# Kernel tuning notes

Hardware: AMD Instinct MI355X
Metric: run time of the kernel (lower is better)

The kernel has to match this reference:

```python
import jax, jax.numpy as jnp
import numpy as np

B, N, C, H = 8, 1025, 1024, 16


def setup_inputs() -> dict:
    key = jax.random.key(0)
    k1, k2, k3, k4 = jax.random.split(key, 4)
    x = jax.random.normal(k1, (B, N, C), dtype=jnp.float32)
    w_qkv = jax.random.normal(k2, (3 * C, C), dtype=jnp.float32) * (C ** -0.5)
    w_proj = jax.random.normal(k3, (C, C), dtype=jnp.float32) * (C ** -0.5)
    b_proj = jax.random.normal(k4, (C,), dtype=jnp.float32) * 0.01
    return {"x": x, "w_qkv": w_qkv, "w_proj": w_proj, "b_proj": b_proj}


def reference(x, w_qkv, w_proj, b_proj):
    b, n, c = x.shape
    hd = c // H
    scale = hd ** -0.5
    qkv = (x @ w_qkv.T).reshape(b, n, 3, H, hd).transpose(2, 0, 3, 1, 4)
    q, k, v = qkv[0], qkv[1], qkv[2]
    # standard QK attention path
    attn_ori = jax.nn.softmax(jnp.einsum('bhnd,bhmd->bhnm', q, k) * scale, axis=-1)
    # CLIP-Surgery V-V self-correlation path (settings='' -> same scale)
    attn_vv = jax.nn.softmax(jnp.einsum('bhnd,bhmd->bhnm', v, v) * scale, axis=-1)
    x_ori = jnp.einsum('bhnm,bhmd->bhnd', attn_ori, v).transpose(0, 2, 1, 3).reshape(b, n, c)
    x_new = jnp.einsum('bhnm,bhmd->bhnd', attn_vv, v).transpose(0, 2, 1, 3).reshape(b, n, c)
    out_vv = x_new @ w_proj.T + b_proj
    out_ori = x_ori @ w_proj.T + b_proj
    return (out_vv, out_ori)
```

## Files before the change

### kernel.cpp

```cpp
#include <hip/hip_runtime.h>

typedef unsigned short ushort_t;
typedef __attribute__((ext_vector_type(8))) __bf16 bf16x8;
typedef __attribute__((ext_vector_type(4))) float f32x4;

constexpr int B_ = 8, N_ = 1025, C_ = 1024, H_ = 16, HD = 64;
constexpr int M_QKV = B_ * N_;
constexpr int M_PROJ = 2 * B_ * N_;
constexpr int K_ = 1024;
constexpr int NT = 1032;
constexpr size_t S1 = (size_t)B_ * H_ * N_ * HD;
constexpr size_t VT_SZ = (size_t)B_ * H_ * HD * NT;

__device__ __forceinline__ ushort_t f2bf(float f) {
    union { float f; unsigned u; } a; a.f = f;
    unsigned r = a.u + 0x7FFFu + ((a.u >> 16) & 1u);
    return (ushort_t)(r >> 16);
}
__device__ __forceinline__ unsigned pk2(float x, float y) {
    unsigned a = __float_as_uint(x) + 0x8000u;
    unsigned b = __float_as_uint(y) + 0x8000u;
    return (a >> 16) | (b & 0xffff0000u);
}
__device__ __forceinline__ uint4 pack8(float4 x, float4 y) {
    return make_uint4(pk2(x.x, x.y), pk2(x.z, x.w), pk2(y.x, y.y), pk2(y.z, y.w));
}

union U4 { uint4 v; ushort_t s[8]; };

__device__ __forceinline__ void gload16(const ushort_t* g, ushort_t* l) {
    __builtin_amdgcn_global_load_lds(
        (const __attribute__((address_space(1))) void*)g,
        (__attribute__((address_space(3))) void*)l, 16, 0, 0);
}

__global__ __launch_bounds__(256)
void conv_bf16(const float* __restrict__ src, ushort_t* __restrict__ dst, int n8) {
    const int i = blockIdx.x * 256 + threadIdx.x;
    if (i < n8) {
        const float4* s = (const float4*)src + 2 * (size_t)i;
        ((uint4*)dst)[i] = pack8(s[0], s[1]);
    }
}

__global__ __launch_bounds__(256)
void gemm_qkv(const ushort_t* __restrict__ A, const ushort_t* __restrict__ Bm,
              ushort_t* __restrict__ q, ushort_t* __restrict__ k,
              ushort_t* __restrict__ v, ushort_t* __restrict__ vT) {
    const int lin = blockIdx.x;
    const int xcd = lin & 7;
    const int j = lin >> 3;
    const int m_local = j % 9;
    const int n_idx = j / 9;
    const int m_idx = xcd * 9 + m_local;
    if (m_idx >= 65) return;
    const int m0 = m_idx * 128, n0 = n_idx * 128;

    __shared__ ushort_t As[128 * 32];
    __shared__ ushort_t Bs[128 * 32];
    const int tid = threadIdx.x;
    const int wave = tid >> 6, lane = tid & 63;
    const int quad = lane >> 4, l16 = lane & 15;
    const int wm = (wave & 1) * 64, wn = (wave >> 1) * 64;

    const int col8 = (tid & 3) * 8;
    const int row0 = tid >> 2;
    const int ar0 = min(m0 + row0,      M_QKV - 1);
    const int ar1 = min(m0 + row0 + 64, M_QKV - 1);
    const ushort_t* ga0 = A + (size_t)ar0 * K_ + col8;
    const ushort_t* ga1 = A + (size_t)ar1 * K_ + col8;
    const ushort_t* gb0 = Bm + (size_t)(n0 + row0) * K_ + col8;
    const ushort_t* gb1 = Bm + (size_t)(n0 + row0 + 64) * K_ + col8;
    ushort_t* lA0 = As + tid * 8;
    ushort_t* lA1 = As + (tid + 256) * 8;
    ushort_t* lB0 = Bs + tid * 8;
    ushort_t* lB1 = Bs + (tid + 256) * 8;

    f32x4 acc[4][4] = {};

    for (int k0 = 0; k0 < K_; k0 += 32) {
        __syncthreads();
        gload16(ga0 + k0, lA0);
        gload16(ga1 + k0, lA1);
        gload16(gb0 + k0, lB0);
        gload16(gb1 + k0, lB1);
        __syncthreads();
        bf16x8 af[4], bfr[4];
#pragma unroll
        for (int i = 0; i < 4; i++) {
            af[i]  = *(const bf16x8*)(As + (wm + i * 16 + l16) * 32 + quad * 8);
            bfr[i] = *(const bf16x8*)(Bs + (wn + i * 16 + l16) * 32 + quad * 8);
        }
#pragma unroll
        for (int im = 0; im < 4; im++)
#pragma unroll
            for (int in = 0; in < 4; in++)
                acc[im][in] = __builtin_amdgcn_mfma_f32_16x16x32_bf16(af[im], bfr[in], acc[im][in], 0, 0, 0);
    }

#pragma unroll
    for (int im = 0; im < 4; im++) {
#pragma unroll
        for (int in = 0; in < 4; in++) {
            const int gcol = n0 + wn + in * 16 + l16;
            const int which = gcol >> 10;
            const int c = gcol & 1023;
            const int h = c >> 6, d = c & 63;
            ushort_t* dst = which == 0 ? q : (which == 1 ? k : v);
            const float sc = (which == 0) ? 0.125f : 1.0f;
#pragma unroll
            for (int r = 0; r < 4; r++) {
                const int grow = m0 + wm + im * 16 + quad * 4 + r;
                if (grow < M_QKV) {
                    const int b = grow / N_;
                    const int nn = grow - b * N_;
                    const ushort_t val = f2bf(acc[im][in][r] * sc);
                    const size_t bh = (size_t)(b * H_ + h);
                    dst[(bh * N_ + nn) * HD + d] = val;
                    if (which == 2)
                        vT[(bh * HD + d) * NT + nn] = val;
                }
            }
        }
    }
}

__global__ __launch_bounds__(512, 4)
void attn_kernel(const ushort_t* __restrict__ q, const ushort_t* __restrict__ k,
                 const ushort_t* __restrict__ v, const ushort_t* __restrict__ vT,
                 ushort_t* __restrict__ xvv, ushort_t* __restrict__ xori) {
    __shared__ ushort_t Kd[2][64 * 64];
    __shared__ ushort_t Vd[2][64 * 64];
    __shared__ ushort_t Td[2][64 * 64];
    __shared__ ushort_t Ps[8 * 16 * 64];

    const int tid = threadIdx.x;
    const int wave = tid >> 6, lane = tid & 63;
    const int quad = lane >> 4, l16 = lane & 15;

    const int lin = blockIdx.x;
    const int r8 = lin & 7;
    const int j = lin >> 3;
    const int g = j / 9;
    const int qt = j - g * 9;
    const int bh = g * 8 + r8;
    const int b = bh >> 4, h = bh & 15;

    const size_t base  = (size_t)bh * N_ * HD;
    const size_t baseT = (size_t)bh * HD * NT;
    const int qstart = min(qt * 128, N_ - 128);
    const int qr0 = qstart + wave * 16;

    const int swz  = (l16 & 7) << 3;
    const int a7   = l16 & 7;
    const int prow = (wave * 16 + l16) * 64;
    const int kq4  = quad * 4;

    const int srow = tid >> 3;
    const int scol = 8 * ((tid & 7) ^ (srow & 7));
    const int ld = tid * 8;

    bf16x8 qq[2], qv[2];
    {
        const int qrow = qr0 + l16;
#pragma unroll
        for (int kk = 0; kk < 2; kk++) {
            U4 uq, uv;
            uq.v = *(const uint4*)(q + base + (size_t)qrow * HD + kk * 32 + quad * 8);
            uv.v = *(const uint4*)(v + base + (size_t)qrow * HD + kk * 32 + quad * 8);
            qq[kk] = *(const bf16x8*)uq.s;
            qv[kk] = *(const bf16x8*)uv.s;
        }
    }

    float l0 = 0.f, l1 = 0.f;
    f32x4 o0[4] = {}, o1[4] = {};

    const int nkt = (N_ + 63) / 64;

    gload16(k + base + (size_t)srow * HD + scol,   &Kd[0][ld]);
    gload16(v + base + (size_t)srow * HD + scol,   &Vd[0][ld]);
    gload16(vT + baseT + (size_t)srow * NT + scol, &Td[0][ld]);

    for (int kt = 0; kt < nkt; kt++) {
        const int key0 = kt * 64;
        const bool tail = (key0 + 64 > N_);
        const int cur = kt & 1;

        __syncthreads();

        if (kt + 1 < nkt) {
            const int kn = key0 + 64;
            const int nb = cur ^ 1;
            const int kk0 = min(kn + srow, N_ - 1);
            gload16(k + base + (size_t)kk0 * HD + scol, &Kd[nb][ld]);
            gload16(v + base + (size_t)kk0 * HD + scol, &Vd[nb][ld]);
            gload16(vT + baseT + (size_t)srow * NT + kn + scol, &Td[nb][ld]);
        }

        const ushort_t* Kc = Kd[cur];
        const ushort_t* Vc = Vd[cur];
        const ushort_t* Tc = Td[cur];

        f32x4 s[4];
        __builtin_amdgcn_s_setprio(1);
#pragma unroll
        for (int t = 0; t < 4; t++) {
            const int row = (t * 16 + l16) * 64;
            bf16x8 b0 = *(const bf16x8*)(Kc + row + ((quad * 8) ^ swz));
            bf16x8 b1 = *(const bf16x8*)(Kc + row + ((32 + quad * 8) ^ swz));
            f32x4 a = {};
            a = __builtin_amdgcn_mfma_f32_16x16x32_bf16(b0, qq[0], a, 0, 0, 0);
            a = __builtin_amdgcn_mfma_f32_16x16x32_bf16(b1, qq[1], a, 0, 0, 0);
            s[t] = a;
        }
        __builtin_amdgcn_s_setprio(0);

        if (tail) {
#pragma unroll
            for (int t = 0; t < 4; t++)
#pragma unroll
                for (int r = 0; r < 4; r++)
                    if (key0 + t * 16 + kq4 + r >= N_) s[t][r] = -1e30f;
        }
#pragma unroll
        for (int t = 0; t < 4; t++) {
            const float p0 = __expf(s[t][0]);
            const float p1 = __expf(s[t][1]);
            const float p2 = __expf(s[t][2]);
            const float p3 = __expf(s[t][3]);
            l0 += (p0 + p1) + (p2 + p3);
            *(uint2*)(&Ps[prow + (((t * 4 + quad) >> 1) ^ a7) * 8 + (quad & 1) * 4]) =
                make_uint2(pk2(p0, p1), pk2(p2, p3));
        }
        {
            bf16x8 pa0 = *(const bf16x8*)(&Ps[prow + ((quad    ) ^ a7) * 8]);
            bf16x8 pa1 = *(const bf16x8*)(&Ps[prow + ((quad + 4) ^ a7) * 8]);
            __builtin_amdgcn_s_setprio(1);
#pragma unroll
            for (int t = 0; t < 4; t++) {
                const int row = (t * 16 + l16) * 64;
                bf16x8 bv0 = *(const bf16x8*)(Tc + row + ((quad * 8) ^ swz));
                bf16x8 bv1 = *(const bf16x8*)(Tc + row + ((32 + quad * 8) ^ swz));
                o0[t] = __builtin_amdgcn_mfma_f32_16x16x32_bf16(pa0, bv0, o0[t], 0, 0, 0);
                o0[t] = __builtin_amdgcn_mfma_f32_16x16x32_bf16(pa1, bv1, o0[t], 0, 0, 0);
            }
            __builtin_amdgcn_s_setprio(0);
        }

        __builtin_amdgcn_s_setprio(1);
#pragma unroll
        for (int t = 0; t < 4; t++) {
            const int row = (t * 16 + l16) * 64;
            bf16x8 b0 = *(const bf16x8*)(Vc + row + ((quad * 8) ^ swz));
            bf16x8 b1 = *(const bf16x8*)(Vc + row + ((32 + quad * 8) ^ swz));
            f32x4 a = {};
            a = __builtin_amdgcn_mfma_f32_16x16x32_bf16(b0, qv[0], a, 0, 0, 0);
            a = __builtin_amdgcn_mfma_f32_16x16x32_bf16(b1, qv[1], a, 0, 0, 0);
            s[t] = a;
        }
        __builtin_amdgcn_s_setprio(0);
        if (tail) {
#pragma unroll
            for (int t = 0; t < 4; t++)
#pragma unroll
                for (int r = 0; r < 4; r++)
                    if (key0 + t * 16 + kq4 + r >= N_) s[t][r] = -1e30f;
        }
#pragma unroll
        for (int t = 0; t < 4; t++) {
            const float p0 = __expf(s[t][0] * 0.125f);
            const float p1 = __expf(s[t][1] * 0.125f);
            const float p2 = __expf(s[t][2] * 0.125f);
            const float p3 = __expf(s[t][3] * 0.125f);
            l1 += (p0 + p1) + (p2 + p3);
            *(uint2*)(&Ps[prow + (((t * 4 + quad) >> 1) ^ a7) * 8 + (quad & 1) * 4]) =
                make_uint2(pk2(p0, p1), pk2(p2, p3));
        }
        {
            bf16x8 pa0 = *(const bf16x8*)(&Ps[prow + ((quad    ) ^ a7) * 8]);
            bf16x8 pa1 = *(const bf16x8*)(&Ps[prow + ((quad + 4) ^ a7) * 8]);
            __builtin_amdgcn_s_setprio(1);
#pragma unroll
            for (int t = 0; t < 4; t++) {
                const int row = (t * 16 + l16) * 64;
                bf16x8 bv0 = *(const bf16x8*)(Tc + row + ((quad * 8) ^ swz));
                bf16x8 bv1 = *(const bf16x8*)(Tc + row + ((32 + quad * 8) ^ swz));
                o1[t] = __builtin_amdgcn_mfma_f32_16x16x32_bf16(pa0, bv0, o1[t], 0, 0, 0);
                o1[t] = __builtin_amdgcn_mfma_f32_16x16x32_bf16(pa1, bv1, o1[t], 0, 0, 0);
            }
            __builtin_amdgcn_s_setprio(0);
        }
    }

    l0 += __shfl_xor(l0, 16);
    l0 += __shfl_xor(l0, 32);
    l1 += __shfl_xor(l1, 16);
    l1 += __shfl_xor(l1, 32);
#pragma unroll
    for (int r = 0; r < 4; r++) {
        const float inv0 = 1.0f / __shfl(l0, kq4 + r);
        const float inv1 = 1.0f / __shfl(l1, kq4 + r);
        const int row = qr0 + kq4 + r;
        const size_t rb = (size_t)(b * N_ + row) * C_ + h * HD;
#pragma unroll
        for (int t = 0; t < 4; t++) {
            const int d = t * 16 + l16;
            xori[rb + d] = f2bf(o0[t][r] * inv0);
            xvv[rb + d]  = f2bf(o1[t][r] * inv1);
        }
    }
}

__global__ __launch_bounds__(256)
void gemm_proj(const ushort_t* __restrict__ A, const ushort_t* __restrict__ Bm,
               const float* __restrict__ bias, float* __restrict__ out) {
    const int lin = blockIdx.x;
    const int xcd = lin & 7;
    const int j = lin >> 3;
    const int m_local = j % 17;
    const int n_idx = j / 17;
    const int m_idx = xcd * 17 + m_local;
    if (m_idx >= 129) return;
    const int m0 = m_idx * 128, n0 = n_idx * 128;

    __shared__ ushort_t As[128 * 32];
    __shared__ ushort_t Bs[128 * 32];
    const int tid = threadIdx.x;
    const int wave = tid >> 6, lane = tid & 63;
    const int quad = lane >> 4, l16 = lane & 15;
    const int wm = (wave & 1) * 64, wn = (wave >> 1) * 64;

    const int col8 = (tid & 3) * 8;
    const int row0 = tid >> 2;
    const int ar0 = min(m0 + row0,      M_PROJ - 1);
    const int ar1 = min(m0 + row0 + 64, M_PROJ - 1);
    const ushort_t* ga0 = A + (size_t)ar0 * K_ + col8;
    const ushort_t* ga1 = A + (size_t)ar1 * K_ + col8;
    const ushort_t* gb0 = Bm + (size_t)(n0 + row0) * K_ + col8;
    const ushort_t* gb1 = Bm + (size_t)(n0 + row0 + 64) * K_ + col8;
    ushort_t* lA0 = As + tid * 8;
    ushort_t* lA1 = As + (tid + 256) * 8;
    ushort_t* lB0 = Bs + tid * 8;
    ushort_t* lB1 = Bs + (tid + 256) * 8;

    f32x4 acc[4][4] = {};

    for (int k0 = 0; k0 < K_; k0 += 32) {
        __syncthreads();
        gload16(ga0 + k0, lA0);
        gload16(ga1 + k0, lA1);
        gload16(gb0 + k0, lB0);
        gload16(gb1 + k0, lB1);
        __syncthreads();
        bf16x8 af[4], bfr[4];
#pragma unroll
        for (int i = 0; i < 4; i++) {
            af[i]  = *(const bf16x8*)(As + (wm + i * 16 + l16) * 32 + quad * 8);
            bfr[i] = *(const bf16x8*)(Bs + (wn + i * 16 + l16) * 32 + quad * 8);
        }
#pragma unroll
        for (int im = 0; im < 4; im++)
#pragma unroll
            for (int in = 0; in < 4; in++)
                acc[im][in] = __builtin_amdgcn_mfma_f32_16x16x32_bf16(af[im], bfr[in], acc[im][in], 0, 0, 0);
    }

#pragma unroll
    for (int im = 0; im < 4; im++) {
#pragma unroll
        for (int in = 0; in < 4; in++) {
            const int gcol = n0 + wn + in * 16 + l16;
            const float bb = bias[gcol];
#pragma unroll
            for (int r = 0; r < 4; r++) {
                const int grow = m0 + wm + im * 16 + quad * 4 + r;
                if (grow < M_PROJ)
                    out[(size_t)grow * C_ + gcol] = acc[im][in][r] + bb;
            }
        }
    }
}

extern "C" void kernel_launch(void* const* d_in, const int* in_sizes, int n_in,
                              void* d_out, int out_size, void* d_ws, size_t ws_size,
                              hipStream_t stream) {
    const float* x      = (const float*)d_in[0];
    const float* w_qkv  = (const float*)d_in[1];
    const float* w_proj = (const float*)d_in[2];
    const float* b_proj = (const float*)d_in[3];
    float* out = (float*)d_out;

    ushort_t* ws = (ushort_t*)d_ws;
    ushort_t* x_bf     = ws;
    ushort_t* xvv      = ws;
    ushort_t* xori     = ws + S1;
    ushort_t* v        = ws + 2 * S1;
    ushort_t* wproj_bf = ws + 2 * S1;

    ushort_t* q        = (ushort_t*)d_out;
    ushort_t* k        = (ushort_t*)d_out + S1;
    ushort_t* vT       = (ushort_t*)d_out + 2 * S1;
    ushort_t* wqkv_bf  = (ushort_t*)d_out + 2 * S1 + VT_SZ;

    {
        const int n8x = (int)(S1 / 8);
        conv_bf16<<<(n8x + 255) / 256, 256, 0, stream>>>(x, x_bf, n8x);
        const int n8w = 3 * C_ * C_ / 8;
        conv_bf16<<<(n8w + 255) / 256, 256, 0, stream>>>(w_qkv, wqkv_bf, n8w);
    }
    {
        gemm_qkv<<<dim3(8 * 24 * 9), 256, 0, stream>>>(x_bf, wqkv_bf, q, k, v, vT);
    }
    {
        attn_kernel<<<dim3(9 * B_ * H_), 512, 0, stream>>>(q, k, v, vT, xvv, xori);
    }
    {
        const int n8p = C_ * C_ / 8;
        conv_bf16<<<(n8p + 255) / 256, 256, 0, stream>>>(w_proj, wproj_bf, n8p);
    }
    {
        gemm_proj<<<dim3(8 * 8 * 17), 256, 0, stream>>>(xvv, wproj_bf, b_proj, out);
    }
}
```

Baseline: 378.7 us.

## Double-buffer LDS tiles in QKV and projection GEMMs to overlap loads with MFMA

Replaces the single-buffer load-sync-compute K loop in both GEMM kernels with a two-stage LDS ping-pong pipeline. The next K slice is issued via global_load_lds while the current slice is computed, using explicit vmcnt waits and barriers. This targets the global-load latency that was fully exposed each iteration. It doubles LDS use per block, which may reduce occupancy, and relies on hand-placed waitcnt counts being correct.

```diff
diff --git a/kernel.cpp b/kernel.cpp
--- a/kernel.cpp
+++ b/kernel.cpp
@@ -42,6 +42,54 @@
         ((uint4*)dst)[i] = pack8(s[0], s[1]);
     }
 }
+
+__device__ __forceinline__ void gemm_stage(const ushort_t* ga0, const ushort_t* ga1,
+                                           const ushort_t* gb0, const ushort_t* gb1,
+                                           ushort_t* As, ushort_t* Bs,
+                                           int ld0, int ld1, int kk) {
+    gload16(ga0 + kk, As + ld0);
+    gload16(ga1 + kk, As + ld1);
+    gload16(gb0 + kk, Bs + ld0);
+    gload16(gb1 + kk, Bs + ld1);
+}
+
+__device__ __forceinline__ void gemm_compute(const ushort_t* As, const ushort_t* Bs,
+                                             int wm, int wn, int l16, int quad,
+                                             f32x4 (&acc)[4][4]) {
+    bf16x8 af[4], bfr[4];
+#pragma unroll
+    for (int i = 0; i < 4; i++) {
+        af[i]  = *(const bf16x8*)(As + (wm + i * 16 + l16) * 32 + quad * 8);
+        bfr[i] = *(const bf16x8*)(Bs + (wn + i * 16 + l16) * 32 + quad * 8);
+    }
+#pragma unroll
+    for (int im = 0; im < 4; im++)
+#pragma unroll
+        for (int in = 0; in < 4; in++)
+            acc[im][in] = __builtin_amdgcn_mfma_f32_16x16x32_bf16(af[im], bfr[in], acc[im][in], 0, 0, 0);
+}
+
+#define GEMM_KLOOP(As0_, Bs0_, As1_, Bs1_)                                     \
+    gemm_stage(ga0, ga1, gb0, gb1, As0_, Bs0_, ld0, ld1, 0);                   \
+    _Pragma("unroll 1")                                                        \
+    for (int t = 0; t < 32; t += 2) {                                          \
+        gemm_stage(ga0, ga1, gb0, gb1, As1_, Bs1_, ld0, ld1, (t + 1) * 32);    \
+        asm volatile("s_waitcnt vmcnt(4)" ::: "memory");                       \
+        __builtin_amdgcn_s_barrier();                                          \
+        __builtin_amdgcn_sched_barrier(0);                                     \
+        gemm_compute(As0_, Bs0_, wm, wn, l16, quad, acc);                      \
+        __builtin_amdgcn_s_barrier();                                          \
+        if (t + 2 < 32) {                                                      \
+            gemm_stage(ga0, ga1, gb0, gb1, As0_, Bs0_, ld0, ld1, (t + 2) * 32);\
+            asm volatile("s_waitcnt vmcnt(4)" ::: "memory");                   \
+        } else {                                                               \
+            asm volatile("s_waitcnt vmcnt(0)" ::: "memory");                   \
+        }                                                                      \
+        __builtin_amdgcn_s_barrier();                                          \
+        __builtin_amdgcn_sched_barrier(0);                                     \
+        gemm_compute(As1_, Bs1_, wm, wn, l16, quad, acc);                      \
+        __builtin_amdgcn_s_barrier();                                          \
+    }
 
 __global__ __launch_bounds__(256)
 void gemm_qkv(const ushort_t* __restrict__ A, const ushort_t* __restrict__ Bm,
@@ -56,8 +104,8 @@
     if (m_idx >= 65) return;
     const int m0 = m_idx * 128, n0 = n_idx * 128;
 
-    __shared__ ushort_t As[128 * 32];
-    __shared__ ushort_t Bs[128 * 32];
+    __shared__ ushort_t As0[128 * 32], Bs0[128 * 32];
+    __shared__ ushort_t As1[128 * 32], Bs1[128 * 32];
     const int tid = threadIdx.x;
     const int wave = tid >> 6, lane = tid & 63;
     const int quad = lane >> 4, l16 = lane & 15;
@@ -71,32 +119,11 @@
     const ushort_t* ga1 = A + (size_t)ar1 * K_ + col8;
     const ushort_t* gb0 = Bm + (size_t)(n0 + row0) * K_ + col8;
     const ushort_t* gb1 = Bm + (size_t)(n0 + row0 + 64) * K_ + col8;
-    ushort_t* lA0 = As + tid * 8;
-    ushort_t* lA1 = As + (tid + 256) * 8;
-    ushort_t* lB0 = Bs + tid * 8;
-    ushort_t* lB1 = Bs + (tid + 256) * 8;
+    const int ld0 = tid * 8, ld1 = (tid + 256) * 8;
 
     f32x4 acc[4][4] = {};
 
-    for (int k0 = 0; k0 < K_; k0 += 32) {
-        __syncthreads();
-        gload16(ga0 + k0, lA0);
-        gload16(ga1 + k0, lA1);
-        gload16(gb0 + k0, lB0);
-        gload16(gb1 + k0, lB1);
-        __syncthreads();
-        bf16x8 af[4], bfr[4];
-#pragma unroll
-        for (int i = 0; i < 4; i++) {
-            af[i]  = *(const bf16x8*)(As + (wm + i * 16 + l16) * 32 + quad * 8);
-            bfr[i] = *(const bf16x8*)(Bs + (wn + i * 16 + l16) * 32 + quad * 8);
-        }
-#pragma unroll
-        for (int im = 0; im < 4; im++)
-#pragma unroll
-            for (int in = 0; in < 4; in++)
-                acc[im][in] = __builtin_amdgcn_mfma_f32_16x16x32_bf16(af[im], bfr[in], acc[im][in], 0, 0, 0);
-    }
+    GEMM_KLOOP(As0, Bs0, As1, Bs1)
 
 #pragma unroll
     for (int im = 0; im < 4; im++) {
@@ -324,8 +351,8 @@
     if (m_idx >= 129) return;
     const int m0 = m_idx * 128, n0 = n_idx * 128;
 
-    __shared__ ushort_t As[128 * 32];
-    __shared__ ushort_t Bs[128 * 32];
+    __shared__ ushort_t As0[128 * 32], Bs0[128 * 32];
+    __shared__ ushort_t As1[128 * 32], Bs1[128 * 32];
     const int tid = threadIdx.x;
     const int wave = tid >> 6, lane = tid & 63;
     const int quad = lane >> 4, l16 = lane & 15;
@@ -339,32 +366,11 @@
     const ushort_t* ga1 = A + (size_t)ar1 * K_ + col8;
     const ushort_t* gb0 = Bm + (size_t)(n0 + row0) * K_ + col8;
     const ushort_t* gb1 = Bm + (size_t)(n0 + row0 + 64) * K_ + col8;
-    ushort_t* lA0 = As + tid * 8;
-    ushort_t* lA1 = As + (tid + 256) * 8;
-    ushort_t* lB0 = Bs + tid * 8;
-    ushort_t* lB1 = Bs + (tid + 256) * 8;
+    const int ld0 = tid * 8, ld1 = (tid + 256) * 8;
 
     f32x4 acc[4][4] = {};
 
-    for (int k0 = 0; k0 < K_; k0 += 32) {
-        __syncthreads();
-        gload16(ga0 + k0, lA0);
-        gload16(ga1 + k0, lA1);
-        gload16(gb0 + k0, lB0);
-        gload16(gb1 + k0, lB1);
-        __syncthreads();
-        bf16x8 af[4], bfr[4];
-#pragma unroll
-        for (int i = 0; i < 4; i++) {
-            af[i]  = *(const bf16x8*)(As + (wm + i * 16 + l16) * 32 + quad * 8);
-            bfr[i] = *(const bf16x8*)(Bs + (wn + i * 16 + l16) * 32 + quad * 8);
-        }
-#pragma unroll
-        for (int im = 0; im < 4; im++)
-#pragma unroll
-            for (int in = 0; in < 4; in++)
-                acc[im][in] = __builtin_amdgcn_mfma_f32_16x16x32_bf16(af[im], bfr[in], acc[im][in], 0, 0, 0);
-    }
+    GEMM_KLOOP(As0, Bs0, As1, Bs1)
 
 #pragma unroll
     for (int im = 0; im < 4; im++) {
```

New measurement: 385.0 us. No clear change (+1.7%).
